# Optimization experiments

Measured on AMD Instinct MI355X. Metric: run time of the kernel, lower is better.

## Reference

```python
import jax, jax.numpy as jnp
import numpy as np
from jax import lax

N, P, Z, L = 1000, 50000, 10, 5


def setup_inputs() -> dict:
    key = jax.random.key(0)
    ks = jax.random.split(key, 9)
    data = jax.random.normal(ks[0], (N, P), dtype=jnp.float32)
    mean_z = jax.random.normal(ks[1], (N, Z), dtype=jnp.float32)
    A = jax.random.normal(ks[2], (Z, Z), dtype=jnp.float32) * 0.1
    var_z = A @ A.T + 0.01 * jnp.eye(Z, dtype=jnp.float32)  # PSD
    mean_w = jax.random.normal(ks[3], (L, Z, P), dtype=jnp.float32) * 0.01
    var_w = jax.random.uniform(ks[4], (L, Z), dtype=jnp.float32) + 0.1   # positive
    alpha = jax.nn.softmax(jax.random.normal(ks[5], (L, Z, P), dtype=jnp.float32), axis=-1)
    tau_0 = jax.random.uniform(ks[6], (L, Z), dtype=jnp.float32) + 0.5   # positive prior precision
    pi = jax.nn.softmax(jax.random.normal(ks[7], (Z, P), dtype=jnp.float32), axis=-1)
    tau = jnp.array(1.0, dtype=jnp.float32)
    return dict(data=data, mean_z=mean_z, var_z=var_z, mean_w=mean_w,
                var_w=var_w, alpha=alpha, tau_0=tau_0, pi=pi, tau=tau)


def _log_bf(z, s2, s0):
    s0_inv = 1.0 / s0
    s2ps0inv = s2 + s0_inv
    return 0.5 * (jnp.log(s2) - jnp.log(s2ps0inv) + z ** 2 * (s0_inv / s2ps0inv))


def reference(data, mean_z, var_z, mean_w, var_w, alpha, tau_0, pi, tau):
    n_dim = data.shape[0]
    l_dim, z_dim, p_dim = mean_w.shape

    # FactorModel.moments
    mean_zz = mean_z.T @ mean_z + n_dim * var_z            # [z, z]
    # LoadingModel.moments (only mean_w moment is needed)
    W0 = jnp.sum(mean_w * alpha, axis=0)                    # [z, p]

    def factor_body(kdx, carry):
        W, mw, vw, al = carry
        not_k = jnp.where(jnp.arange(z_dim) != kdx, size=z_dim - 1)[0]  # [z-1]
        E_zpzk = mean_zz[kdx][not_k]                        # [z-1]
        E_zzk = mean_zz[kdx, kdx]                           # scalar
        Wk = W[kdx]                                         # [p]
        Wnk = W[not_k]                                      # [z-1, p]
        RtZk = mean_z[:, kdx] @ data - Wnk.T @ E_zpzk       # [p]

        def effect_body(ldx, ecarry):
            Wk, mw, vw, al = ecarry
            Wkl = Wk - mw[ldx, kdx] * al[ldx, kdx]          # [p] residualized
            E_RtZk = RtZk - E_zzk * Wkl                     # [p]
            u_var = jnp.reciprocal(tau * E_zzk + tau_0[ldx, kdx])  # scalar
            u_mean = tau * u_var * E_RtZk                   # [p]
            Z_s = E_RtZk / E_zzk * jnp.sqrt(E_zzk * tau)    # [p]
            s2_s = 1.0 / (E_zzk * tau)
            log_bf = _log_bf(Z_s, s2_s, tau_0[ldx, kdx])
            alpha_kl = jax.nn.softmax(jnp.log(pi[kdx]) + log_bf)   # [p]
            Wk_new = Wkl + u_mean * alpha_kl
            return (Wk_new,
                    mw.at[ldx, kdx].set(u_mean),
                    vw.at[ldx, kdx].set(u_var),
                    al.at[ldx, kdx].set(alpha_kl))

        Wk, mw, vw, al = lax.fori_loop(0, l_dim, effect_body, (Wk, mw, vw, al))
        return (W.at[kdx].set(Wk), mw, vw, al)

    W, mw, vw, al = lax.fori_loop(0, z_dim, factor_body, (W0, mean_w, var_w, alpha))
    return mw, vw, al
```

## Files before the change

### kernel.cpp

```cpp
#include <hip/hip_runtime.h>
#include <math.h>

#define N_DIM 1000
#define P_DIM 50000
#define Z_DIM 10
#define L_DIM 5
#define NT 256
#define NB 196
#define NSPLIT 4
#define NCHUNK 250
#define NEG_BIG (-3.0e38f)

constexpr size_t ZP      = (size_t)Z_DIM * P_DIM;
constexpr size_t OFF_ZTR = 0;
constexpr size_t OFF_W   = ZP;
constexpr size_t OFF_WK  = 2 * ZP;
constexpr size_t OFF_RTZ = 2 * ZP + P_DIM;
constexpr size_t OFF_LG  = 2 * ZP + 2 * P_DIM;
constexpr size_t OFF_ZZ  = 2 * ZP + 3 * P_DIM;
constexpr size_t OFF_PM0 = OFF_ZZ + 128;
constexpr size_t OFF_PS0 = OFF_PM0 + NB;
constexpr size_t OFF_PM1 = OFF_PS0 + NB;
constexpr size_t OFF_PS1 = OFF_PM1 + NB;

constexpr size_t OUT_MW = 0;
constexpr size_t OUT_VW = (size_t)L_DIM * Z_DIM * P_DIM;
constexpr size_t OUT_AL = OUT_VW + (size_t)L_DIM * Z_DIM;

__device__ inline void online_merge(float& m, float& e, float m2, float e2) {
    float M = fmaxf(m, m2);
    e = e * __expf(m - M) + e2 * __expf(m2 - M);
    m = M;
}

__device__ inline void block_merge(float& m, float& e, float* sm, float* se, float* bro) {
    int lane = threadIdx.x & 63;
    int wid  = threadIdx.x >> 6;
    #pragma unroll
    for (int off = 32; off > 0; off >>= 1) {
        float m2 = __shfl_xor(m, off);
        float e2 = __shfl_xor(e, off);
        online_merge(m, e, m2, e2);
    }
    if (lane == 0) { sm[wid] = m; se[wid] = e; }
    __syncthreads();
    if (threadIdx.x == 0) {
        float M = sm[0], E = se[0];
        #pragma unroll
        for (int w = 1; w < NT / 64; w++) online_merge(M, E, sm[w], se[w]);
        bro[0] = M; bro[1] = E;
    }
    __syncthreads();
    m = bro[0]; e = bro[1];
}

__global__ __launch_bounds__(256) void init_zz(const float* __restrict__ mean_z,
                                               const float* __restrict__ var_z,
                                               float* __restrict__ ws) {
    float* zz = ws + OFF_ZZ;
    int i = blockIdx.x / Z_DIM, j = blockIdx.x % Z_DIM;
    float s = 0.f;
    for (int n = threadIdx.x; n < N_DIM; n += 256)
        s += mean_z[n * Z_DIM + i] * mean_z[n * Z_DIM + j];
    #pragma unroll
    for (int off = 32; off > 0; off >>= 1) s += __shfl_xor(s, off);
    __shared__ float ls[4];
    if ((threadIdx.x & 63) == 0) ls[threadIdx.x >> 6] = s;
    __syncthreads();
    if (threadIdx.x == 0) {
        float t = ls[0] + ls[1] + ls[2] + ls[3];
        zz[blockIdx.x] = t + (float)N_DIM * var_z[blockIdx.x];
    }
}

__global__ __launch_bounds__(NT) void precompute_big(const float* __restrict__ data,
                                                     const float* __restrict__ mean_z,
                                                     const float* __restrict__ mw0,
                                                     const float* __restrict__ al0,
                                                     float* __restrict__ ws) {
    float* ZtR = ws + OFF_ZTR;
    float* W   = ws + OFF_W;
    __shared__ float mzs[NCHUNK * Z_DIM];
    int n0 = blockIdx.y * NCHUNK;
    for (int i = threadIdx.x; i < NCHUNK * Z_DIM; i += NT)
        mzs[i] = mean_z[n0 * Z_DIM + i];
    __syncthreads();
    int p = blockIdx.x * NT + threadIdx.x;
    if (p >= P_DIM) return;

    float acc[Z_DIM];
    #pragma unroll
    for (int z = 0; z < Z_DIM; z++) acc[z] = 0.f;
    for (int r = 0; r < NCHUNK; r++) {
        float d = data[(size_t)(n0 + r) * P_DIM + p];
        #pragma unroll
        for (int z = 0; z < Z_DIM; z++) acc[z] += mzs[r * Z_DIM + z] * d;
    }
    #pragma unroll
    for (int z = 0; z < Z_DIM; z++) atomicAdd(&ZtR[(size_t)z * P_DIM + p], acc[z]);

    if (blockIdx.y == 0) {
        #pragma unroll
        for (int z = 0; z < Z_DIM; z++) {
            float w = 0.f;
            #pragma unroll
            for (int l = 0; l < L_DIM; l++) {
                size_t io = ((size_t)l * Z_DIM + z) * P_DIM + p;
                w += mw0[io] * al0[io];
            }
            W[(size_t)z * P_DIM + p] = w;
        }
    }
}

__global__ __launch_bounds__(NT) void step_kernel(const float* __restrict__ mw0,
                                                  const float* __restrict__ al0,
                                                  const float* __restrict__ pi,
                                                  const float* __restrict__ tau0,
                                                  const float* __restrict__ taup,
                                                  float* __restrict__ ws,
                                                  float* __restrict__ out,
                                                  int k, int l, int pk, int pl,
                                                  int has_prev, int prev_last, int s) {
    float* ZtR = ws + OFF_ZTR;
    float* W   = ws + OFF_W;
    float* Wk  = ws + OFF_WK;
    float* RtZ = ws + OFF_RTZ;
    float* lg  = ws + OFF_LG;
    float* zz  = ws + OFF_ZZ;
    int wbuf = s & 1, rbuf = 1 - wbuf;
    float* pm_r = ws + (rbuf ? OFF_PM1 : OFF_PM0);
    float* ps_r = ws + (rbuf ? OFF_PS1 : OFF_PS0);
    float* pm_w = ws + (wbuf ? OFF_PM1 : OFF_PM0);
    float* ps_w = ws + (wbuf ? OFF_PS1 : OFF_PS0);

    float* out_mw = out + OUT_MW;
    float* out_vw = out + OUT_VW;
    float* out_al = out + OUT_AL;

    __shared__ float sm[NT / 64], se[NT / 64], bro[2];

    int tid = threadIdx.x;
    int p = blockIdx.x * NT + tid;
    bool valid = p < P_DIM;
    float tau = taup[0];

    float wk = 0.f;

    if (has_prev) {
        float m = NEG_BIG, e = 0.f;
        if (tid < NB) { m = pm_r[tid]; e = ps_r[tid]; }
        block_merge(m, e, sm, se, bro);
        float M = m, S = e;
        if (valid) {
            float a = __expf(lg[p] - M) / S;
            size_t po = ((size_t)pl * Z_DIM + pk) * P_DIM + p;
            out_al[po] = a;
            float um = out_mw[po];
            wk = Wk[p] + um * a;
            if (prev_last) W[(size_t)pk * P_DIM + p] = wk;
        }
    }

    float Ezz   = zz[k * Z_DIM + k];
    float t0v   = tau0[l * Z_DIM + k];
    float u_var = 1.f / (tau * Ezz + t0v);
    float s2    = 1.f / (Ezz * tau);
    float s0inv = 1.f / t0v;
    float cq    = 0.5f * (tau / Ezz) * (s0inv / (s2 + s0inv));

    float r = 0.f;
    if (valid) {
        if (l == 0) {
            r = ZtR[(size_t)k * P_DIM + p];
            #pragma unroll
            for (int j = 0; j < Z_DIM; j++) {
                if (j == k) continue;
                float wj = (has_prev && prev_last && j == pk) ? wk
                                                              : W[(size_t)j * P_DIM + p];
                r -= zz[k * Z_DIM + j] * wj;
            }
            RtZ[p] = r;
            wk = W[(size_t)k * P_DIM + p];
        } else {
            r = RtZ[p];
        }
    }

    float m = NEG_BIG, e = 0.f;
    if (valid) {
        size_t io = ((size_t)l * Z_DIM + k) * P_DIM + p;
        float wkl = wk - mw0[io] * al0[io];
        float E   = r - Ezz * wkl;
        float um  = tau * u_var * E;
        float lgt = __logf(pi[(size_t)k * P_DIM + p]) + cq * E * E;
        out_mw[io] = um;
        lg[p] = lgt;
        Wk[p] = wkl;
        m = lgt; e = 1.f;
    }
    block_merge(m, e, sm, se, bro);
    if (tid == 0) { pm_w[blockIdx.x] = m; ps_w[blockIdx.x] = e; }
    if (tid == 0 && blockIdx.x == 0) out_vw[l * Z_DIM + k] = u_var;
}

__global__ __launch_bounds__(NT) void final_kernel(float* __restrict__ ws,
                                                   float* __restrict__ out, int s_last) {
    float* lg = ws + OFF_LG;
    int rbuf = s_last & 1;
    float* pm_r = ws + (rbuf ? OFF_PM1 : OFF_PM0);
    float* ps_r = ws + (rbuf ? OFF_PS1 : OFF_PS0);
    float* out_al = out + OUT_AL;

    __shared__ float sm[NT / 64], se[NT / 64], bro[2];
    int tid = threadIdx.x;
    int p = blockIdx.x * NT + tid;

    float m = NEG_BIG, e = 0.f;
    if (tid < NB) { m = pm_r[tid]; e = ps_r[tid]; }
    block_merge(m, e, sm, se, bro);
    if (p < P_DIM) {
        float a = __expf(lg[p] - m) / e;
        out_al[((size_t)4 * Z_DIM + 9) * P_DIM + p] = a;
    }
}

extern "C" void kernel_launch(void* const* d_in, const int* in_sizes, int n_in,
                              void* d_out, int out_size, void* d_ws, size_t ws_size,
                              hipStream_t stream) {
    (void)in_sizes; (void)n_in; (void)out_size; (void)ws_size;
    const float* data   = (const float*)d_in[0];
    const float* mean_z = (const float*)d_in[1];
    const float* var_z  = (const float*)d_in[2];
    const float* mw0    = (const float*)d_in[3];
    const float* al0    = (const float*)d_in[5];
    const float* tau0   = (const float*)d_in[6];
    const float* pi     = (const float*)d_in[7];
    const float* taup   = (const float*)d_in[8];
    float* out = (float*)d_out;
    float* ws  = (float*)d_ws;

    hipMemsetAsync(ws, 0, ZP * sizeof(float), stream);
    init_zz<<<Z_DIM * Z_DIM, 256, 0, stream>>>(mean_z, var_z, ws);
    precompute_big<<<dim3(NB, NSPLIT), NT, 0, stream>>>(data, mean_z, mw0, al0, ws);

    for (int s = 0; s < Z_DIM * L_DIM; s++) {
        int k = s / L_DIM, l = s % L_DIM;
        int pk = (s > 0) ? (s - 1) / L_DIM : 0;
        int pl = (s > 0) ? (s - 1) % L_DIM : 0;
        int has_prev  = (s > 0) ? 1 : 0;
        int prev_last = (has_prev && pl == L_DIM - 1) ? 1 : 0;
        step_kernel<<<NB, NT, 0, stream>>>(mw0, al0, pi, tau0, taup, ws, out,
                                           k, l, pk, pl, has_prev, prev_last, s);
    }
    final_kernel<<<NB, NT, 0, stream>>>(ws, out, Z_DIM * L_DIM - 1);
}
```

Baseline: 574.2 us.

## Fuse 50 sequential step kernels into one persistent kernel with grid barriers

Replaces the 50 per-step kernel launches plus a final kernel with a single persistent kernel of 196 blocks. Each thread keeps its column of W in registers and prefetches the next step's inputs, and blocks exchange softmax partials through a packed 64-bit atomic buffer with a counter-based grid barrier. This removes launch overhead and the global round-trips for Wk, RtZ and lg between steps. It relies on all 196 blocks being co-resident, otherwise the spin barrier deadlocks.

```diff
diff --git a/kernel.cpp b/kernel.cpp
--- a/kernel.cpp
+++ b/kernel.cpp
@@ -9,23 +9,23 @@
 #define NB 196
 #define NSPLIT 4
 #define NCHUNK 250
+#define NSTEPS 50
 #define NEG_BIG (-3.0e38f)
 
 constexpr size_t ZP      = (size_t)Z_DIM * P_DIM;
 constexpr size_t OFF_ZTR = 0;
 constexpr size_t OFF_W   = ZP;
-constexpr size_t OFF_WK  = 2 * ZP;
-constexpr size_t OFF_RTZ = 2 * ZP + P_DIM;
-constexpr size_t OFF_LG  = 2 * ZP + 2 * P_DIM;
-constexpr size_t OFF_ZZ  = 2 * ZP + 3 * P_DIM;
-constexpr size_t OFF_PM0 = OFF_ZZ + 128;
-constexpr size_t OFF_PS0 = OFF_PM0 + NB;
-constexpr size_t OFF_PM1 = OFF_PS0 + NB;
-constexpr size_t OFF_PS1 = OFF_PM1 + NB;
-
-constexpr size_t OUT_MW = 0;
+constexpr size_t OFF_ZZ  = 2 * ZP;
+constexpr size_t OFF_CNT = 2 * ZP + 128;
+constexpr size_t OFF_PART= OFF_CNT + 64;
+
 constexpr size_t OUT_VW = (size_t)L_DIM * Z_DIM * P_DIM;
 constexpr size_t OUT_AL = OUT_VW + (size_t)L_DIM * Z_DIM;
+
+__device__ inline unsigned long long pack2(float m, float e) {
+    return (unsigned long long)__float_as_uint(m) |
+           ((unsigned long long)__float_as_uint(e) << 32);
+}
 
 __device__ inline void online_merge(float& m, float& e, float m2, float e2) {
     float M = fmaxf(m, m2);
@@ -113,115 +113,114 @@
     }
 }
 
-__global__ __launch_bounds__(NT) void step_kernel(const float* __restrict__ mw0,
+__global__ __launch_bounds__(NT) void fused_steps(const float* __restrict__ mw0,
                                                   const float* __restrict__ al0,
                                                   const float* __restrict__ pi,
                                                   const float* __restrict__ tau0,
                                                   const float* __restrict__ taup,
                                                   float* __restrict__ ws,
-                                                  float* __restrict__ out,
-                                                  int k, int l, int pk, int pl,
-                                                  int has_prev, int prev_last, int s) {
+                                                  float* __restrict__ out) {
     float* ZtR = ws + OFF_ZTR;
-    float* W   = ws + OFF_W;
-    float* Wk  = ws + OFF_WK;
-    float* RtZ = ws + OFF_RTZ;
-    float* lg  = ws + OFF_LG;
+    float* Wg  = ws + OFF_W;
     float* zz  = ws + OFF_ZZ;
-    int wbuf = s & 1, rbuf = 1 - wbuf;
-    float* pm_r = ws + (rbuf ? OFF_PM1 : OFF_PM0);
-    float* ps_r = ws + (rbuf ? OFF_PS1 : OFF_PS0);
-    float* pm_w = ws + (wbuf ? OFF_PM1 : OFF_PM0);
-    float* ps_w = ws + (wbuf ? OFF_PS1 : OFF_PS0);
-
-    float* out_mw = out + OUT_MW;
+    unsigned int* cnt       = (unsigned int*)(ws + OFF_CNT);
+    unsigned long long* part= (unsigned long long*)(ws + OFF_PART);
+
+    float* out_mw = out;
     float* out_vw = out + OUT_VW;
     float* out_al = out + OUT_AL;
 
     __shared__ float sm[NT / 64], se[NT / 64], bro[2];
 
     int tid = threadIdx.x;
-    int p = blockIdx.x * NT + tid;
+    int blk = blockIdx.x;
+    int p = blk * NT + tid;
     bool valid = p < P_DIM;
     float tau = taup[0];
 
-    float wk = 0.f;
-
-    if (has_prev) {
-        float m = NEG_BIG, e = 0.f;
-        if (tid < NB) { m = pm_r[tid]; e = ps_r[tid]; }
-        block_merge(m, e, sm, se, bro);
-        float M = m, S = e;
-        if (valid) {
-            float a = __expf(lg[p] - M) / S;
-            size_t po = ((size_t)pl * Z_DIM + pk) * P_DIM + p;
-            out_al[po] = a;
-            float um = out_mw[po];
-            wk = Wk[p] + um * a;
-            if (prev_last) W[(size_t)pk * P_DIM + p] = wk;
-        }
-    }
-
-    float Ezz   = zz[k * Z_DIM + k];
-    float t0v   = tau0[l * Z_DIM + k];
-    float u_var = 1.f / (tau * Ezz + t0v);
-    float s2    = 1.f / (Ezz * tau);
-    float s0inv = 1.f / t0v;
-    float cq    = 0.5f * (tau / Ezz) * (s0inv / (s2 + s0inv));
-
-    float r = 0.f;
+    float W[Z_DIM];
+    #pragma unroll
+    for (int z = 0; z < Z_DIM; z++)
+        W[z] = valid ? Wg[(size_t)z * P_DIM + p] : 0.f;
+
+    float nx_mw = 0.f, nx_al = 0.f, nx_ztr = 0.f, nx_pi = 1.f;
     if (valid) {
+        nx_mw  = mw0[p];
+        nx_al  = al0[p];
+        nx_ztr = ZtR[p];
+        nx_pi  = pi[p];
+    }
+
+    float wk = 0.f, r = 0.f, lp = 0.f;
+    int k = 0, l = 0;
+    for (int s = 0; s < NSTEPS; s++) {
+        float Ezz   = zz[k * Z_DIM + k];
+        float t0v   = tau0[l * Z_DIM + k];
+        float u_var = 1.f / (tau * Ezz + t0v);
+        float s2    = 1.f / (Ezz * tau);
+        float s0inv = 1.f / t0v;
+        float cq    = 0.5f * (tau / Ezz) * (s0inv / (s2 + s0inv));
+
         if (l == 0) {
-            r = ZtR[(size_t)k * P_DIM + p];
+            r = nx_ztr;
             #pragma unroll
-            for (int j = 0; j < Z_DIM; j++) {
-                if (j == k) continue;
-                float wj = (has_prev && prev_last && j == pk) ? wk
-                                                              : W[(size_t)j * P_DIM + p];
-                r -= zz[k * Z_DIM + j] * wj;
-            }
-            RtZ[p] = r;
-            wk = W[(size_t)k * P_DIM + p];
-        } else {
-            r = RtZ[p];
-        }
-    }
-
-    float m = NEG_BIG, e = 0.f;
-    if (valid) {
+            for (int j = 0; j < Z_DIM; j++)
+                if (j != k) r -= zz[k * Z_DIM + j] * W[j];
+            wk = W[k];
+            lp = __logf(nx_pi);
+        }
+
         size_t io = ((size_t)l * Z_DIM + k) * P_DIM + p;
-        float wkl = wk - mw0[io] * al0[io];
+        float wkl = wk - nx_mw * nx_al;
         float E   = r - Ezz * wkl;
         float um  = tau * u_var * E;
-        float lgt = __logf(pi[(size_t)k * P_DIM + p]) + cq * E * E;
-        out_mw[io] = um;
-        lg[p] = lgt;
-        Wk[p] = wkl;
-        m = lgt; e = 1.f;
-    }
-    block_merge(m, e, sm, se, bro);
-    if (tid == 0) { pm_w[blockIdx.x] = m; ps_w[blockIdx.x] = e; }
-    if (tid == 0 && blockIdx.x == 0) out_vw[l * Z_DIM + k] = u_var;
-}
-
-__global__ __launch_bounds__(NT) void final_kernel(float* __restrict__ ws,
-                                                   float* __restrict__ out, int s_last) {
-    float* lg = ws + OFF_LG;
-    int rbuf = s_last & 1;
-    float* pm_r = ws + (rbuf ? OFF_PM1 : OFF_PM0);
-    float* ps_r = ws + (rbuf ? OFF_PS1 : OFF_PS0);
-    float* out_al = out + OUT_AL;
-
-    __shared__ float sm[NT / 64], se[NT / 64], bro[2];
-    int tid = threadIdx.x;
-    int p = blockIdx.x * NT + tid;
-
-    float m = NEG_BIG, e = 0.f;
-    if (tid < NB) { m = pm_r[tid]; e = ps_r[tid]; }
-    block_merge(m, e, sm, se, bro);
-    if (p < P_DIM) {
-        float a = __expf(lg[p] - m) / e;
-        out_al[((size_t)4 * Z_DIM + 9) * P_DIM + p] = a;
+        float lgt = valid ? (lp + cq * E * E) : NEG_BIG;
+        if (valid) out_mw[io] = um;
+        if (blk == 0 && tid == 0) out_vw[l * Z_DIM + k] = u_var;
+
+        float m = lgt, e = valid ? 1.f : 0.f;
+        block_merge(m, e, sm, se, bro);
+
+        int l2 = l + 1, k2 = k;
+        if (l2 == L_DIM) { l2 = 0; k2++; }
+        if (s + 1 < NSTEPS && valid) {
+            size_t io2 = ((size_t)l2 * Z_DIM + k2) * P_DIM + p;
+            nx_mw = mw0[io2];
+            nx_al = al0[io2];
+            if (l2 == 0) {
+                nx_ztr = ZtR[(size_t)k2 * P_DIM + p];
+                nx_pi  = pi[(size_t)k2 * P_DIM + p];
+            }
+        }
+
+        unsigned long long* pbuf = part + (size_t)(s & 1) * NB;
+        if (tid == 0) {
+            __hip_atomic_store(&pbuf[blk], pack2(m, e),
+                               __ATOMIC_RELAXED, __HIP_MEMORY_SCOPE_AGENT);
+            __hip_atomic_fetch_add(&cnt[s], 1u,
+                                   __ATOMIC_RELEASE, __HIP_MEMORY_SCOPE_AGENT);
+            while (__hip_atomic_load(&cnt[s], __ATOMIC_ACQUIRE,
+                                     __HIP_MEMORY_SCOPE_AGENT) < (unsigned)NB)
+                __builtin_amdgcn_s_sleep(1);
+        }
+        __syncthreads();
+
+        float mm = NEG_BIG, ee = 0.f;
+        if (tid < NB) {
+            unsigned long long v = __hip_atomic_load(&pbuf[tid], __ATOMIC_ACQUIRE,
+                                                     __HIP_MEMORY_SCOPE_AGENT);
+            mm = __uint_as_float((unsigned)v);
+            ee = __uint_as_float((unsigned)(v >> 32));
+        }
+        block_merge(mm, ee, sm, se, bro);
+
+        if (valid) {
+            float a = __expf(lgt - mm) / ee;
+            out_al[io] = a;
+            wk = wkl + um * a;
+            if (l == L_DIM - 1) W[k] = wk;
+        }
+        l = l2; k = k2;
     }
 }
 
@@ -241,17 +240,9 @@
     float* ws  = (float*)d_ws;
 
     hipMemsetAsync(ws, 0, ZP * sizeof(float), stream);
+    hipMemsetAsync((char*)d_ws + OFF_CNT * sizeof(float), 0, 64 * sizeof(unsigned int), stream);
+
     init_zz<<<Z_DIM * Z_DIM, 256, 0, stream>>>(mean_z, var_z, ws);
     precompute_big<<<dim3(NB, NSPLIT), NT, 0, stream>>>(data, mean_z, mw0, al0, ws);
-
-    for (int s = 0; s < Z_DIM * L_DIM; s++) {
-        int k = s / L_DIM, l = s % L_DIM;
-        int pk = (s > 0) ? (s - 1) / L_DIM : 0;
-        int pl = (s > 0) ? (s - 1) % L_DIM : 0;
-        int has_prev  = (s > 0) ? 1 : 0;
-        int prev_last = (has_prev && pl == L_DIM - 1) ? 1 : 0;
-        step_kernel<<<NB, NT, 0, stream>>>(mw0, al0, pi, tau0, taup, ws, out,
-                                           k, l, pk, pl, has_prev, prev_last, s);
-    }
-    final_kernel<<<NB, NT, 0, stream>>>(ws, out, Z_DIM * L_DIM - 1);
-}
+    fused_steps<<<NB, NT, 0, stream>>>(mw0, al0, pi, tau0, taup, ws, out);
+}
```

New measurement: 1.164 ms. 2.03x slower.
